# Kernel tuning notes

Hardware: AMD Instinct MI355X
Metric: run time of the kernel (lower is better)

The kernel has to match this reference:

```python
import jax, jax.numpy as jnp
import numpy as np

B = 8192
N = 2048  # output_dim; input_dim = 4*N


def setup_inputs() -> dict:
    key = jax.random.key(0)
    k1, k2, k3, k4, k5 = jax.random.split(key, 5)
    weight = jax.random.normal(k1, (B, 4 * N), dtype=jnp.float32)
    fc_w = jax.random.normal(k2, (N, 4 * N), dtype=jnp.float32) * 0.02
    fc_b = jax.random.normal(k3, (N,), dtype=jnp.float32) * 0.02
    # per-sample coin flips (torch.rand(1) < 0.5), precomputed as constants
    swap1 = jax.random.randint(k4, (B,), 0, 2, dtype=jnp.int32)
    swap2 = jax.random.randint(k5, (B,), 0, 2, dtype=jnp.int32)
    return {"weight": weight, "fc_w": fc_w, "fc_b": fc_b, "swap1": swap1, "swap2": swap2}


def _permute_rows(x, swap1, swap2):
    # x: [B, 4, n]. Sequential swaps: first swap rows (1,2) if swap1, then
    # swap rows (2,3) (of the already-swapped tensor) if swap2.
    s1 = swap1.astype(bool)
    s2 = swap2.astype(bool)
    r0 = jnp.zeros_like(swap1)
    r1 = jnp.where(s1, 2, 1)
    mid = jnp.where(s1, 1, 2)  # what sits at row 2 after swap1
    r2 = jnp.where(s2, 3, mid)
    r3 = jnp.where(s2, mid, 3)
    perm = jnp.stack([r0, r1, r2, r3], axis=1)  # [B, 4]
    return jnp.take_along_axis(x, perm[:, :, None], axis=1)


def reference(weight, fc_w, fc_b, swap1, swap2):
    b = weight.shape[0]
    n = fc_w.shape[0]
    x = weight.reshape(b, 4, n)
    x = _permute_rows(x, swap1, swap2)
    x = x.reshape(b, 4 * n)
    return x @ fc_w.T + fc_b
```

## Files before the change

### kernel.cpp

```cpp
#include <hip/hip_runtime.h>
#include <hip/hip_bf16.h>
#include <stdint.h>


using f32x4   = __attribute__((ext_vector_type(4))) float;
using bf16x8  = __attribute__((ext_vector_type(8))) __bf16;
using ushort8 = __attribute__((ext_vector_type(8))) unsigned short;

#define B_ROWS 8192
#define K_TOT  8192
#define N_OUT  2048
#define BK     64
#define NT     (K_TOT / BK)

__device__ __forceinline__ unsigned short f2bf(float f) {
  union { float f; unsigned int u; } v;
  v.f = f;
  unsigned int r = v.u + 0x7FFFu + ((v.u >> 16) & 1u);
  return (unsigned short)(r >> 16);
}

__device__ __forceinline__ int perm_src(int r, int s1, int s2) {
  int mid = s1 ? 1 : 2;
  return (r == 0) ? 0
       : (r == 1) ? (s1 ? 2 : 1)
       : (r == 2) ? (s2 ? 3 : mid)
                  : (s2 ? mid : 3);
}

__global__ __launch_bounds__(256) void k_prep(
    const float* __restrict__ w, const int* __restrict__ s1v,
    const int* __restrict__ s2v, const float* __restrict__ fw,
    unsigned short* __restrict__ xbf, unsigned short* __restrict__ wbf) {
  const int blk = blockIdx.x;
  const float* src;
  unsigned short* dst;
  if (blk < B_ROWS * 4) {
    const int b = blk >> 2, r = blk & 3;
    const int s1 = s1v[b] != 0, s2 = s2v[b] != 0;
    const int pr = perm_src(r, s1, s2);
    src = w + (size_t)b * K_TOT + (size_t)pr * 2048 + threadIdx.x * 8;
    dst = xbf + (size_t)b * K_TOT + (size_t)r * 2048 + threadIdx.x * 8;
  } else {
    const size_t base = ((size_t)(blk - B_ROWS * 4) * 256 + threadIdx.x) * 8;
    src = fw + base;
    dst = wbf + base;
  }
  f32x4 v0 = *(const f32x4*)src;
  f32x4 v1 = *(const f32x4*)(src + 4);
  ushort8 o;
#pragma unroll
  for (int j = 0; j < 4; ++j) o[j] = f2bf(v0[j]);
#pragma unroll
  for (int j = 0; j < 4; ++j) o[4 + j] = f2bf(v1[j]);
  *(ushort8*)dst = o;
}

__device__ __forceinline__ void gload16(const unsigned short* g,
                                        const unsigned short* l) {
  __builtin_amdgcn_global_load_lds(
      (__attribute__((address_space(1))) void*)(uintptr_t)(const void*)g,
      (__attribute__((address_space(3))) void*)(unsigned int)(uintptr_t)(const void*)l,
      16, 0, 0);
}


#define VMW4 asm volatile("s_waitcnt vmcnt(4)" ::: "memory")
#define VMW0 asm volatile("s_waitcnt vmcnt(0)" ::: "memory")
#define VMWN ((void)0)
#define LGKM0_FENCE do { \
    asm volatile("s_waitcnt lgkmcnt(0)" ::: "memory"); \
    __builtin_amdgcn_sched_barrier(0); } while (0)

#define LDA(BU, MH, M, KKI) \
  (*(const bf16x8*)(smb + (BU)*65536 + aBase + ((MH)*64 + (M)*16)*128 + colsw[KKI]))
#define LDB(BU, NH, N, KKI) \
  (*(const bf16x8*)(smb + (BU)*65536 + 32768 + bBase + ((NH)*32 + (N)*16)*128 + colsw[KKI]))

#define STAGE(BU, OPL, GOP, H, T) do { \
  gload16((GOP) + (size_t)((H)*128 + row0) * K_TOT + (size_t)(T)*BK + sl0, \
          smu + (BU)*32768 + (OPL) + (H)*8192 + tid*8); \
  gload16((GOP) + (size_t)((H)*128 + row1) * K_TOT + (size_t)(T)*BK + sl1, \
          smu + (BU)*32768 + (OPL) + (H)*8192 + 4096 + tid*8); \
} while (0)

#define QUAD(MH, NH, B0A, B1A) do { \
  _Pragma("unroll") for (int m_ = 0; m_ < 4; ++m_) \
    _Pragma("unroll") for (int n_ = 0; n_ < 2; ++n_) { \
      acc[(MH)*4+m_][(NH)*2+n_] = __builtin_amdgcn_mfma_f32_16x16x32_bf16( \
          aR0[m_], B0A[n_], acc[(MH)*4+m_][(NH)*2+n_], 0, 0, 0); \
      acc[(MH)*4+m_][(NH)*2+n_] = __builtin_amdgcn_mfma_f32_16x16x32_bf16( \
          aR1[m_], B1A[n_], acc[(MH)*4+m_][(NH)*2+n_], 0, 0, 0); \
    } \
} while (0)

#define TILE(BU, T, DOA, DOB, WAIT) do { \
  _Pragma("unroll") for (int m_ = 0; m_ < 4; ++m_) { \
    aR0[m_] = LDA(BU, 0, m_, 0); aR1[m_] = LDA(BU, 0, m_, 1); } \
  _Pragma("unroll") for (int n_ = 0; n_ < 2; ++n_) { \
    bL0[n_] = LDB(BU, 0, n_, 0); bL1[n_] = LDB(BU, 0, n_, 1); } \
  if (DOA) STAGE((BU) ^ 1, 0, gA, 0, (T) + 1); \
  __builtin_amdgcn_s_barrier(); \
  LGKM0_FENCE; \
  __builtin_amdgcn_s_setprio(1); QUAD(0, 0, bL0, bL1); __builtin_amdgcn_s_setprio(0); \
  __builtin_amdgcn_s_barrier(); \
  _Pragma("unroll") for (int n_ = 0; n_ < 2; ++n_) { \
    bH0[n_] = LDB(BU, 1, n_, 0); bH1[n_] = LDB(BU, 1, n_, 1); } \
  if (DOA) STAGE((BU) ^ 1, 0, gA, 1, (T) + 1); \
  __builtin_amdgcn_s_barrier(); \
  LGKM0_FENCE; \
  __builtin_amdgcn_s_setprio(1); QUAD(0, 1, bH0, bH1); __builtin_amdgcn_s_setprio(0); \
  __builtin_amdgcn_s_barrier(); \
  _Pragma("unroll") for (int m_ = 0; m_ < 4; ++m_) { \
    aR0[m_] = LDA(BU, 1, m_, 0); aR1[m_] = LDA(BU, 1, m_, 1); } \
  if (DOB) STAGE(BU, 16384, gB, 0, (T) + 2); \
  __builtin_amdgcn_s_barrier(); \
  LGKM0_FENCE; \
  __builtin_amdgcn_s_setprio(1); QUAD(1, 0, bL0, bL1); __builtin_amdgcn_s_setprio(0); \
  __builtin_amdgcn_s_barrier(); \
  if (DOB) STAGE(BU, 16384, gB, 1, (T) + 2); \
  __builtin_amdgcn_s_barrier(); \
  __builtin_amdgcn_s_setprio(1); QUAD(1, 1, bH0, bH1); __builtin_amdgcn_s_setprio(0); \
  WAIT; \
  __builtin_amdgcn_s_barrier(); \
} while (0)

__global__ __launch_bounds__(512, 2) void k_gemm8(
    const unsigned short* __restrict__ A,
    const unsigned short* __restrict__ Bw,
    const float* __restrict__ bias,
    float* __restrict__ C) {
  __shared__ unsigned short sm[2 * 32768];
  unsigned short* smu = sm;
  const char* smb = (const char*)sm;

  const int tid  = threadIdx.x;
  const int lane = tid & 63;
  const int wave = tid >> 6;
  const int wr = wave >> 2;
  const int wc = wave & 3;
  const int g  = blockIdx.x & 7;
  const int bm = g * 4 + ((blockIdx.x >> 3) & 3);
  const int bn = blockIdx.x >> 5;

  const unsigned short* gA = A  + (size_t)bm * 256 * K_TOT;
  const unsigned short* gB = Bw + (size_t)bn * 256 * K_TOT;

  const int row0 = tid >> 3;
  const int sl0  = (((tid & 7) ^ (row0 & 7)) << 3);
  const int row1 = (512 + tid) >> 3;
  const int sl1  = ((((512 + tid) & 7) ^ (row1 & 7)) << 3);

  const int l15 = lane & 15;
  int colsw[2];
  colsw[0] = (((lane >> 4) << 4)) ^ ((lane & 7) << 4);
  colsw[1] = (64 | ((lane >> 4) << 4)) ^ ((lane & 7) << 4);
  const int aBase = (wr * 128 + l15) * 128;
  const int bBase = (wc * 64 + l15) * 128;

  f32x4 acc[8][4];
#pragma unroll
  for (int i = 0; i < 8; ++i)
#pragma unroll
    for (int j = 0; j < 4; ++j) {
      acc[i][j][0] = 0.f; acc[i][j][1] = 0.f; acc[i][j][2] = 0.f; acc[i][j][3] = 0.f;
    }
  bf16x8 aR0[4], aR1[4], bL0[2], bL1[2], bH0[2], bH1[2];

  STAGE(0, 0,     gA, 0, 0);
  STAGE(0, 0,     gA, 1, 0);
  STAGE(0, 16384, gB, 0, 0);
  STAGE(0, 16384, gB, 1, 0);
  STAGE(1, 16384, gB, 0, 1);
  STAGE(1, 16384, gB, 1, 1);
  VMW4;
  __builtin_amdgcn_s_barrier();

  int t = 0;
  for (; t < NT - 4; t += 2) {
    TILE(0, t,     true, true, VMW4);
    TILE(1, t + 1, true, true, VMW4);
  }
  TILE(0, 124, true,  true,  VMW4);
  TILE(1, 125, true,  true,  VMW4);
  TILE(0, 126, true,  false, VMW0);
  TILE(1, 127, false, false, VMWN);

  const int crow0 = bm * 256 + wr * 128 + ((lane >> 4) << 2);
  const int ccol0 = bn * 256 + wc * 64 + l15;
  float bv[4];
#pragma unroll
  for (int n = 0; n < 4; ++n) bv[n] = bias[ccol0 + n * 16];
#pragma unroll
  for (int mi = 0; mi < 8; ++mi)
#pragma unroll
    for (int ni = 0; ni < 4; ++ni) {
      const int r = crow0 + mi * 16;
      const int c = ccol0 + ni * 16;
#pragma unroll
      for (int j = 0; j < 4; ++j)
        C[(size_t)(r + j) * N_OUT + c] = acc[mi][ni][j] + bv[ni];
    }
}

__global__ __launch_bounds__(256) void k_gemm_fallback(
    const float* __restrict__ W, const float* __restrict__ FW,
    const float* __restrict__ bias, const int* __restrict__ s1v,
    const int* __restrict__ s2v, float* __restrict__ C) {
  __shared__ float As[64][33];
  __shared__ float Bs[64][33];
  const int tid = threadIdx.x;
  const int tx = tid & 15, ty = tid >> 4;
  const int bm = blockIdx.x & 127;
  const int bn = blockIdx.x >> 7;
  float acc[4][4] = {{0.f}};
  for (int k0 = 0; k0 < K_TOT; k0 += 32) {
#pragma unroll
    for (int i = 0; i < 8; ++i) {
      int idx = i * 256 + tid;
      int rr = idx >> 5, cc = idx & 31;
      int grow = bm * 64 + rr;
      int gk = k0 + cc;
      int blkr = gk >> 11, within = gk & 2047;
      int s1 = s1v[grow] != 0, s2 = s2v[grow] != 0;
      int pr = perm_src(blkr, s1, s2);
      As[rr][cc] = W[(size_t)grow * K_TOT + (size_t)pr * 2048 + within];
      Bs[rr][cc] = FW[(size_t)(bn * 64 + rr) * K_TOT + gk];
    }
    __syncthreads();
#pragma unroll 8
    for (int kk = 0; kk < 32; ++kk) {
      float a[4], b[4];
#pragma unroll
      for (int i = 0; i < 4; ++i) a[i] = As[ty * 4 + i][kk];
#pragma unroll
      for (int j = 0; j < 4; ++j) b[j] = Bs[tx * 4 + j][kk];
#pragma unroll
      for (int i = 0; i < 4; ++i)
#pragma unroll
        for (int j = 0; j < 4; ++j) acc[i][j] += a[i] * b[j];
    }
    __syncthreads();
  }
#pragma unroll
  for (int i = 0; i < 4; ++i)
#pragma unroll
    for (int j = 0; j < 4; ++j) {
      int r = bm * 64 + ty * 4 + i, c = bn * 64 + tx * 4 + j;
      C[(size_t)r * N_OUT + c] = acc[i][j] + bias[c];
    }
}

extern "C" void kernel_launch(void* const* d_in, const int* in_sizes, int n_in,
                              void* d_out, int out_size, void* d_ws, size_t ws_size,
                              hipStream_t stream) {
  const float* weight = (const float*)d_in[0];
  const float* fc_w   = (const float*)d_in[1];
  const float* fc_b   = (const float*)d_in[2];
  const int*   swap1  = (const int*)d_in[3];
  const int*   swap2  = (const int*)d_in[4];
  float* out = (float*)d_out;

  const size_t xbf_bytes = (size_t)B_ROWS * K_TOT * 2;
  const size_t wbf_bytes = (size_t)N_OUT * K_TOT * 2;
  if (ws_size >= xbf_bytes + wbf_bytes) {
    unsigned short* xbf = (unsigned short*)d_ws;
    unsigned short* wbf = (unsigned short*)((char*)d_ws + xbf_bytes);
    k_prep<<<B_ROWS * 4 + (N_OUT * K_TOT) / 2048, 256, 0, stream>>>(
        weight, swap1, swap2, fc_w, xbf, wbf);
    k_gemm8<<<32 * 8, 512, 0, stream>>>(xbf, wbf, fc_b, out);
  } else {
    k_gemm_fallback<<<128 * 32, 256, 0, stream>>>(weight, fc_w, fc_b, swap1,
                                                  swap2, out);
  }
}
```

Baseline: 290.7 us.

## Prefetch next-tile B fragments during last quadrant and drop per-tile barriers

Reworks the GEMM main-loop schedule so LDS reads of B fragments are issued ahead and overlap with MFMA quadrants. The next tile's low-half B fragments are prefetched during the previous tile's final quadrant, and the high-half B loads move into the first quadrant. Four of the eight barriers per tile are removed. This is meant to cut LDS-load latency stalls and synchronisation overhead in the inner loop. The cost is more live registers and a tighter ordering between global-to-LDS staging and reads of the other buffer.

```diff
diff --git a/kernel.cpp b/kernel.cpp
--- a/kernel.cpp
+++ b/kernel.cpp
@@ -64,10 +64,10 @@
       16, 0, 0);
 }
 
-
 #define VMW4 asm volatile("s_waitcnt vmcnt(4)" ::: "memory")
 #define VMW0 asm volatile("s_waitcnt vmcnt(0)" ::: "memory")
 #define VMWN ((void)0)
+#define SBAR asm volatile("s_barrier" ::: "memory")
 #define LGKM0_FENCE do { \
     asm volatile("s_waitcnt lgkmcnt(0)" ::: "memory"); \
     __builtin_amdgcn_sched_barrier(0); } while (0)
@@ -94,38 +94,43 @@
     } \
 } while (0)
 
-#define TILE(BU, T, DOA, DOB, WAIT) do { \
+#define TILE_N(BU, T, DOA, DOB, WV, DOPF) do { \
   _Pragma("unroll") for (int m_ = 0; m_ < 4; ++m_) { \
     aR0[m_] = LDA(BU, 0, m_, 0); aR1[m_] = LDA(BU, 0, m_, 1); } \
-  _Pragma("unroll") for (int n_ = 0; n_ < 2; ++n_) { \
-    bL0[n_] = LDB(BU, 0, n_, 0); bL1[n_] = LDB(BU, 0, n_, 1); } \
   if (DOA) STAGE((BU) ^ 1, 0, gA, 0, (T) + 1); \
-  __builtin_amdgcn_s_barrier(); \
+  SBAR; \
   LGKM0_FENCE; \
-  __builtin_amdgcn_s_setprio(1); QUAD(0, 0, bL0, bL1); __builtin_amdgcn_s_setprio(0); \
-  __builtin_amdgcn_s_barrier(); \
+  __builtin_amdgcn_s_setprio(1); \
   _Pragma("unroll") for (int n_ = 0; n_ < 2; ++n_) { \
     bH0[n_] = LDB(BU, 1, n_, 0); bH1[n_] = LDB(BU, 1, n_, 1); } \
+  QUAD(0, 0, bL0, bL1); \
+  __builtin_amdgcn_s_setprio(0); \
   if (DOA) STAGE((BU) ^ 1, 0, gA, 1, (T) + 1); \
-  __builtin_amdgcn_s_barrier(); \
+  SBAR; \
   LGKM0_FENCE; \
-  __builtin_amdgcn_s_setprio(1); QUAD(0, 1, bH0, bH1); __builtin_amdgcn_s_setprio(0); \
-  __builtin_amdgcn_s_barrier(); \
+  __builtin_amdgcn_s_setprio(1); \
+  QUAD(0, 1, bH0, bH1); \
+  __builtin_amdgcn_s_setprio(0); \
   _Pragma("unroll") for (int m_ = 0; m_ < 4; ++m_) { \
     aR0[m_] = LDA(BU, 1, m_, 0); aR1[m_] = LDA(BU, 1, m_, 1); } \
   if (DOB) STAGE(BU, 16384, gB, 0, (T) + 2); \
-  __builtin_amdgcn_s_barrier(); \
+  SBAR; \
   LGKM0_FENCE; \
-  __builtin_amdgcn_s_setprio(1); QUAD(1, 0, bL0, bL1); __builtin_amdgcn_s_setprio(0); \
-  __builtin_amdgcn_s_barrier(); \
+  __builtin_amdgcn_s_setprio(1); \
+  QUAD(1, 0, bL0, bL1); \
+  __builtin_amdgcn_s_setprio(0); \
   if (DOB) STAGE(BU, 16384, gB, 1, (T) + 2); \
-  __builtin_amdgcn_s_barrier(); \
-  __builtin_amdgcn_s_setprio(1); QUAD(1, 1, bH0, bH1); __builtin_amdgcn_s_setprio(0); \
-  WAIT; \
-  __builtin_amdgcn_s_barrier(); \
+  WV; \
+  SBAR; \
+  __builtin_amdgcn_s_setprio(1); \
+  if (DOPF) { \
+    _Pragma("unroll") for (int n_ = 0; n_ < 2; ++n_) { \
+      bL0[n_] = LDB((BU) ^ 1, 0, n_, 0); bL1[n_] = LDB((BU) ^ 1, 0, n_, 1); } } \
+  QUAD(1, 1, bH0, bH1); \
+  __builtin_amdgcn_s_setprio(0); \
 } while (0)
 
-__global__ __launch_bounds__(512, 2) void k_gemm8(
+__global__ __launch_bounds__(512, 2) void k_gemm11(
     const unsigned short* __restrict__ A,
     const unsigned short* __restrict__ Bw,
     const float* __restrict__ bias,
@@ -173,18 +178,21 @@
   STAGE(0, 16384, gB, 1, 0);
   STAGE(1, 16384, gB, 0, 1);
   STAGE(1, 16384, gB, 1, 1);
-  VMW4;
-  __builtin_amdgcn_s_barrier();
-
-  int t = 0;
-  for (; t < NT - 4; t += 2) {
-    TILE(0, t,     true, true, VMW4);
-    TILE(1, t + 1, true, true, VMW4);
-  }
-  TILE(0, 124, true,  true,  VMW4);
-  TILE(1, 125, true,  true,  VMW4);
-  TILE(0, 126, true,  false, VMW0);
-  TILE(1, 127, false, false, VMWN);
+  VMW0;
+  SBAR;
+#pragma unroll
+  for (int n_ = 0; n_ < 2; ++n_) {
+    bL0[n_] = LDB(0, 0, n_, 0); bL1[n_] = LDB(0, 0, n_, 1);
+  }
+
+  for (int t = 0; t < 124; t += 2) {
+    TILE_N(0, t,     true, true, VMW4, true);
+    TILE_N(1, t + 1, true, true, VMW4, true);
+  }
+  TILE_N(0, 124, true,  true,  VMW4, true);
+  TILE_N(1, 125, true,  true,  VMW4, true);
+  TILE_N(0, 126, true,  false, VMW0, true);
+  TILE_N(1, 127, false, false, VMWN, false);
 
   const int crow0 = bm * 256 + wr * 128 + ((lane >> 4) << 2);
   const int ccol0 = bn * 256 + wc * 64 + l15;
@@ -268,7 +276,7 @@
     unsigned short* wbf = (unsigned short*)((char*)d_ws + xbf_bytes);
     k_prep<<<B_ROWS * 4 + (N_OUT * K_TOT) / 2048, 256, 0, stream>>>(
         weight, swap1, swap2, fc_w, xbf, wbf);
-    k_gemm8<<<32 * 8, 512, 0, stream>>>(xbf, wbf, fc_b, out);
+    k_gemm11<<<32 * 8, 512, 0, stream>>>(xbf, wbf, fc_b, out);
   } else {
     k_gemm_fallback<<<128 * 32, 256, 0, stream>>>(weight, fc_w, fc_b, swap1,
                                                   swap2, out);
```

New measurement: 281.1 us, median of 2. -3.3%, faster.
